# Kernel optimization log

Measured on AMD Instinct MI355X. Metric: run time of the kernel, lower is better.

## Reference

```python
import jax, jax.numpy as jnp
import numpy as np

FILTER_WIDTH = 32
SEQ_LEN = 4096
BATCH = 128
CHANNELS = 4


def setup_inputs() -> dict:
    key = jax.random.key(0)
    x = jax.random.normal(key, (BATCH, SEQ_LEN, CHANNELS), dtype=jnp.float32)
    return {"x": x}


def reference(x):
    # Unfold seq dim into overlapping windows: [B, L, C] -> [B, L-F+1, F, C]
    n_windows = SEQ_LEN - FILTER_WIDTH + 1  # 4065
    # idx[w, f] = w + f : gather indices for each window position
    idx = jnp.arange(n_windows)[:, None] + jnp.arange(FILTER_WIDTH)[None, :]
    # Single strided gather along axis 1 (im2col-style), replacing the
    # original per-slice loop + concat + reshape.
    return x[:, idx, :]  # [B, n_windows, F, C]
```

## Files before the change

### kernel.cpp

```cpp
#include <hip/hip_runtime.h>


constexpr int FILTER_WIDTH = 32;
constexpr int SEQ_LEN      = 4096;
constexpr int NWIN         = SEQ_LEN - FILTER_WIDTH + 1;
constexpr int BATCH        = 128;
constexpr long long TOTAL4 = (long long)BATCH * NWIN * FILTER_WIDTH;

__global__ void im2col_gather(const float4* __restrict__ x,
                              float4* __restrict__ out,
                              int total) {
    int idx    = blockIdx.x * blockDim.x + threadIdx.x;
    int stride = gridDim.x * blockDim.x;
    for (int o = idx; o < total; o += stride) {
        int f  = o & (FILTER_WIDTH - 1);
        int bw = o >> 5;
        int w  = bw % NWIN;
        int b  = bw / NWIN;
        out[o] = x[(long long)b * SEQ_LEN + w + f];
    }
}

extern "C" void kernel_launch(void* const* d_in, const int* in_sizes, int n_in,
                              void* d_out, int out_size, void* d_ws, size_t ws_size,
                              hipStream_t stream) {
    const float4* x = (const float4*)d_in[0];
    float4* out     = (float4*)d_out;

    const int total = (int)TOTAL4;
    const int block = 256;
    int grid = (total + block - 1) / block;
    if (grid > 2048) grid = 2048;

    im2col_gather<<<grid, block, 0, stream>>>(x, out, total);
}
```

Measured before the change: 272.1 us.

## Tile im2col per batch chunk with batched loads and nontemporal stores

Replaces the grid-stride loop, which did a division and modulo per element, with one block per (batch, 32-window chunk). Each thread issues four independent float4 loads up front and then writes them with nontemporal stores. The aim is to remove the index arithmetic, raise memory-level parallelism, and keep the large write-once output from polluting the cache. The cost is a much larger launch grid and a bounds check on the last, partial chunk of each batch.

```diff
diff --git a/kernel.cpp b/kernel.cpp
--- a/kernel.cpp
+++ b/kernel.cpp
@@ -1,36 +1,48 @@
 #include <hip/hip_runtime.h>
 
 
-constexpr int FILTER_WIDTH = 32;
-constexpr int SEQ_LEN      = 4096;
-constexpr int NWIN         = SEQ_LEN - FILTER_WIDTH + 1;
-constexpr int BATCH        = 128;
-constexpr long long TOTAL4 = (long long)BATCH * NWIN * FILTER_WIDTH;
+using f32x4 = __attribute__((ext_vector_type(4))) float;
 
-__global__ void im2col_gather(const float4* __restrict__ x,
-                              float4* __restrict__ out,
-                              int total) {
-    int idx    = blockIdx.x * blockDim.x + threadIdx.x;
-    int stride = gridDim.x * blockDim.x;
-    for (int o = idx; o < total; o += stride) {
-        int f  = o & (FILTER_WIDTH - 1);
-        int bw = o >> 5;
-        int w  = bw % NWIN;
-        int b  = bw / NWIN;
-        out[o] = x[(long long)b * SEQ_LEN + w + f];
+constexpr int F      = 32;
+constexpr int L      = 4096;
+constexpr int NW     = L - F + 1;
+constexpr int NCHUNK = 128;
+
+__global__ __launch_bounds__(256) void im2col_tile(const f32x4* __restrict__ x,
+                                                   f32x4* __restrict__ out) {
+    const int chunk = blockIdx.x & (NCHUNK - 1);
+    const int b     = blockIdx.x >> 7;
+    const int w0    = chunk << 5;
+    const int t     = threadIdx.x;
+
+    const f32x4* __restrict__ xb = x + (long long)b * L;
+    f32x4* __restrict__ ob       = out + ((long long)b * NW + w0) * F;
+
+    f32x4 v[4];
+    bool  ok[4];
+
+    #pragma unroll
+    for (int k = 0; k < 4; ++k) {
+        const int ol   = t + k * 256;
+        const int wloc = ol >> 5;
+        const int f    = ol & (F - 1);
+        ok[k] = (w0 + wloc) < NW;
+        if (ok[k]) v[k] = xb[w0 + wloc + f];
+    }
+
+    #pragma unroll
+    for (int k = 0; k < 4; ++k) {
+        const int ol = t + k * 256;
+        if (ok[k]) __builtin_nontemporal_store(v[k], &ob[ol]);
     }
 }
 
 extern "C" void kernel_launch(void* const* d_in, const int* in_sizes, int n_in,
                               void* d_out, int out_size, void* d_ws, size_t ws_size,
                               hipStream_t stream) {
-    const float4* x = (const float4*)d_in[0];
-    float4* out     = (float4*)d_out;
+    const f32x4* x = (const f32x4*)d_in[0];
+    f32x4* out     = (f32x4*)d_out;
 
-    const int total = (int)TOTAL4;
-    const int block = 256;
-    int grid = (total + block - 1) / block;
-    if (grid > 2048) grid = 2048;
-
-    im2col_gather<<<grid, block, 0, stream>>>(x, out, total);
+    const int grid = 128 * NCHUNK;
+    im2col_tile<<<grid, 256, 0, stream>>>(x, out);
 }
```

Measured after the change: 272.4 us. No clear change (+0.1%).
